# Kernel optimization log

Measured on AMD Instinct MI355X. Metric: run time of the kernel, lower is better.

Reference implementation:

```python
import jax, jax.numpy as jnp
import numpy as np

NUM_LAYERS = 5  # shared parameters across layers


def _crelu(z):
    # complex ReLU: ReLU applied independently to real and imag parts
    return jnp.maximum(z.real, 0.0) + 1j * jnp.maximum(z.imag, 0.0)


def _layer(Habs2, diagH, noise, maxpow, v, ar, dl, rc):
    # ---- u step ----
    # cov: [B,K,1] = |H|^2 @ |v|^2 (sum over last dim keepdim is identity for width-1) + noise
    cov = jnp.sum(Habs2 @ (jnp.abs(v) ** 2), axis=-1, keepdims=True) + noise[..., None]
    u = diagH[..., None] * v / cov  # [B,K,1] complex
    # ---- w step ---- (w_poly=None branch)
    err = 1.0 - jnp.conj(u) * diagH[..., None] * v
    w = 1.0 / err  # [B,K,1] complex
    # ---- v step ----
    v_tilde = jnp.conj(diagH)[..., None] * u * w  # [B,K,1]
    ul = (jnp.abs(u) ** 2) * jnp.abs(w)  # real [B,K,1]
    ul = jnp.sum(jnp.abs(jnp.swapaxes(Habs2, -2, -1) @ ul), axis=-1, keepdims=True)
    mu = jnp.maximum(jnp.abs(v_tilde) / jnp.sqrt(maxpow)[..., None] - ul, 0.0)
    ula = (ul + mu).astype(v_tilde.dtype)
    # ar + diagload branches: [B,K,1,1] @ [1,C] -> [B,K,1,C]
    vt = (v_tilde / ula)[..., None] @ ar + v_tilde[..., None] @ dl
    # nonlin + recombination: [B,K,1,C] @ [C,1] -> [B,K,1,1]
    vt = _crelu(vt) @ rc
    v_new = vt[..., 0]  # [B,K,1]
    # power correction
    cur = jnp.maximum(maxpow[..., None], jnp.abs(v_new) ** 2)
    corr = jnp.minimum(jnp.sqrt(maxpow[..., None] / cur), 1.0)
    return v_new * corr, u, w


def setup_inputs() -> dict:
    key = jax.random.key(0)
    ks = jax.random.split(key, 12)
    B, K, C = 64, 512, 4
    s = 1.0 / np.sqrt(C + 1)
    inp = {
        "h_re": jax.random.normal(ks[0], (B, K, K), jnp.float32),
        "h_im": jax.random.normal(ks[1], (B, K, K), jnp.float32),
        "user_noise_pow": jax.random.uniform(ks[2], (B, K), jnp.float32, 0.1, 1.0),
        "bss_maxpow": jnp.ones((B, K), jnp.float32),
        "v_in_re": jax.random.normal(ks[3], (B, K, 1), jnp.float32) * 0.5,
        "v_in_im": jax.random.normal(ks[4], (B, K, 1), jnp.float32) * 0.5,
        "ar_re": jax.random.normal(ks[5], (1, C), jnp.float32) * s,
        "ar_im": jax.random.normal(ks[6], (1, C), jnp.float32) * s,
        "dl_re": jax.random.normal(ks[7], (1, C), jnp.float32) * s,
        "dl_im": jax.random.normal(ks[8], (1, C), jnp.float32) * s,
        "rc_re": jax.random.normal(ks[9], (C, 1), jnp.float32) * s,
        "rc_im": jax.random.normal(ks[10], (C, 1), jnp.float32) * s,
    }
    return inp


def reference(h_re, h_im, user_noise_pow, bss_maxpow, v_in_re, v_in_im,
              ar_re, ar_im, dl_re, dl_im, rc_re, rc_im):
    H = (h_re + 1j * h_im).astype(jnp.complex64)
    Habs2 = h_re * h_re + h_im * h_im  # |H|^2, real [B,K,K]
    diagH = jnp.diagonal(H, axis1=-2, axis2=-1)  # [B,K]
    v = (v_in_re + 1j * v_in_im).astype(jnp.complex64)
    ar = (ar_re + 1j * ar_im).astype(jnp.complex64)
    dl = (dl_re + 1j * dl_im).astype(jnp.complex64)
    rc = (rc_re + 1j * rc_im).astype(jnp.complex64)
    vs = []
    for _ in range(NUM_LAYERS):
        v, u, w = _layer(Habs2, diagH, user_noise_pow, bss_maxpow, v, ar, dl, rc)
        vs.append(v)
    vstack = jnp.stack(vs, 0)  # [L,B,K,1] complex
    # return real/imag stacked so the output is a real tensor: [L,B,K,1,2]
    return jnp.stack([vstack.real, vstack.imag], axis=-1)
```

## Files before the change

### kernel.cpp

```cpp
#include <hip/hip_runtime.h>

#define B    64
#define K    512
#define C    4
#define NL   5
#define BK   (B*K)
#define ROWS 128
#define NT   1024
#define GRID (B*4)

typedef _Float16 half_t;
typedef _Float16 half8 __attribute__((ext_vector_type(8)));

#define PART_OFF   0
#define VST_OFF    (36*K*4)
#define XSQ_OFF    (VST_OFF + K*8)
#define MPL_OFF    (XSQ_OFF + K*4)
#define NZ_OFF     (MPL_OFF + K*4)
#define DAB_OFF    (NZ_OFF + ROWS*4)
#define SMEM_BYTES (DAB_OFF + ROWS*4)

__device__ __forceinline__ float ld_l3(const float* p) {
    return __uint_as_float(__hip_atomic_load((const unsigned*)p,
        __ATOMIC_RELAXED, __HIP_MEMORY_SCOPE_AGENT));
}
__device__ __forceinline__ void st_l3(float* p, float v) {
    __hip_atomic_store((unsigned*)p, __float_as_uint(v),
        __ATOMIC_RELAXED, __HIP_MEMORY_SCOPE_AGENT);
}
__device__ __forceinline__ void st_l3_2(float2* p, float2 v) {
    unsigned long long u = ((unsigned long long)__float_as_uint(v.y) << 32)
                         | (unsigned long long)__float_as_uint(v.x);
    __hip_atomic_store((unsigned long long*)p, u,
        __ATOMIC_RELAXED, __HIP_MEMORY_SCOPE_AGENT);
}
__device__ __forceinline__ float2 ld_l3_2(const float2* p) {
    unsigned long long u = __hip_atomic_load((const unsigned long long*)p,
        __ATOMIC_RELAXED, __HIP_MEMORY_SCOPE_AGENT);
    return make_float2(__uint_as_float((unsigned)(u & 0xffffffffu)),
                       __uint_as_float((unsigned)(u >> 32)));
}

template <int CTRL, int ROWMASK>
__device__ __forceinline__ float dppadd(float x) {
    int t = __builtin_amdgcn_update_dpp(0, __float_as_int(x), CTRL, ROWMASK,
                                        0xf, true);
    return x + __int_as_float(t);
}
__device__ __forceinline__ float wsum(float x) {
    x = dppadd<0x111, 0xf>(x);
    x = dppadd<0x112, 0xf>(x);
    x = dppadd<0x114, 0xf>(x);
    x = dppadd<0x118, 0xf>(x);
    x = dppadd<0x142, 0xa>(x);
    x = dppadd<0x143, 0xc>(x);
    return __int_as_float(__builtin_amdgcn_readlane(__float_as_int(x), 63));
}

__global__ __launch_bounds__(NT, 4) void k_all(
    const float* __restrict__ hre,  const float* __restrict__ him,
    const float* __restrict__ noise,const float* __restrict__ mp,
    const float* __restrict__ vre,  const float* __restrict__ vim,
    const float* __restrict__ ar_re,const float* __restrict__ ar_im,
    const float* __restrict__ dl_re,const float* __restrict__ dl_im,
    const float* __restrict__ rc_re,const float* __restrict__ rc_im,
    float2* __restrict__ vtilde,
    float*  __restrict__ ulpart,
    unsigned* __restrict__ bar,
    float* __restrict__ out)
{
    extern __shared__ char smem[];
    float*  part = (float*) (smem + PART_OFF);
    float2* vst  = (float2*)(smem + VST_OFF);
    float*  xsq  = (float*) (smem + XSQ_OFF);
    float*  mpl  = (float*) (smem + MPL_OFF);
    float*  nz   = (float*) (smem + NZ_OFF);
    float*  dab  = (float*) (smem + DAB_OFF);

    const int tid  = threadIdx.x;
    const int lane = tid & 63;
    const int w    = tid >> 6;
    const int b    = blockIdx.x & 63;
    const int q    = blockIdx.x >> 6;
    const int j0   = q * ROWS;
    unsigned* qb   = bar + ((unsigned)b << 5);

    if (tid < K) {
        float a = vre[b * K + tid], c2 = vim[b * K + tid];
        vst[tid] = make_float2(a, c2);
        xsq[tid] = a * a + c2 * c2;
        mpl[tid] = mp[b * K + tid];
    } else if (tid < K + ROWS) {
        nz[tid - K] = noise[b * K + j0 + (tid - K)];
    }
    __syncthreads();

    float xq[8];
#pragma unroll
    for (int t = 0; t < 8; ++t) xq[t] = xsq[t * 64 + lane];

    half8 h[8];
    float rs0[8];
    {
        const size_t gb = ((size_t)b * K + j0) * K;
        float ra[2][8], ia[2][8];
#pragma unroll
        for (int t = 0; t < 8; ++t) {
            ra[0][t] = __builtin_nontemporal_load(hre + gb + (size_t)w * K + t * 64 + lane);
            ia[0][t] = __builtin_nontemporal_load(him + gb + (size_t)w * K + t * 64 + lane);
        }
#pragma unroll
        for (int i = 0; i < 8; ++i) {
            const int cur = i & 1, nxt = cur ^ 1;
            if (i < 7) {
                const size_t rb = gb + (size_t)(16 * (i + 1) + w) * K;
#pragma unroll
                for (int t = 0; t < 8; ++t) {
                    ra[nxt][t] = __builtin_nontemporal_load(hre + rb + t * 64 + lane);
                    ia[nxt][t] = __builtin_nontemporal_load(him + rb + t * 64 + lane);
                }
            }
            float s[8], acc = 0.f;
            half8 hh;
#pragma unroll
            for (int t = 0; t < 8; ++t) {
                s[t]  = ra[cur][t] * ra[cur][t] + ia[cur][t] * ia[cur][t];
                hh[t] = (_Float16)s[t];
                acc  += s[t] * xq[t];
            }
            h[i] = hh;
            const int row = 16 * i + w;
            const int j   = j0 + row;
            if (lane == (j & 63)) dab[row] = s[j >> 6];
            rs0[i] = wsum(acc);
        }
    }

    for (int l = 0; l < NL; ++l) {
        const int buf = l & 1;
        float scov[8];
        if (l == 0) {
#pragma unroll
            for (int r = 0; r < 8; ++r) scov[r] = rs0[r];
        } else {
#pragma unroll
            for (int t = 0; t < 8; ++t) xq[t] = xsq[t * 64 + lane];
#pragma unroll
            for (int r = 0; r < 8; ++r) {
                float acc = 0.f;
#pragma unroll
                for (int t = 0; t < 8; ++t) acc += (float)h[r][t] * xq[t];
                scov[r] = wsum(acc);
            }
        }
        float ulv_own = 0.f;
        if (lane < 8) {
            float s = scov[0];
#pragma unroll
            for (int r = 1; r < 8; ++r) s = (lane == r) ? scov[r] : s;
            const int row = 16 * lane + w;
            const int j   = j0 + row;
            const int bj  = b * K + j;
            const float cov = s + nz[row];
            const float d2  = dab[row];
            const float A   = d2 * xsq[j];
            const float ww  = cov / (cov - A);
            const float sc  = d2 * ww / cov;
            const float2 vv = vst[j];
            st_l3_2(&vtilde[buf * BK + bj], make_float2(sc * vv.x, sc * vv.y));
            ulv_own = A * ww / (cov * cov);
        }
        float ulv[8];
#pragma unroll
        for (int r = 0; r < 8; ++r)
            ulv[r] = __int_as_float(
                __builtin_amdgcn_readlane(__float_as_int(ulv_own), r));

#pragma unroll
        for (int t = 0; t < 8; ++t) {
            float a = 0.f;
#pragma unroll
            for (int r = 0; r < 8; ++r) a += (float)h[r][t] * ulv[r];
            part[w * K + t * 64 + lane] = a;
        }
        __syncthreads();

        float s2 = 0.f;
        if (tid < K) {
#pragma unroll
            for (int ws2 = 0; ws2 < 16; ++ws2) s2 += part[ws2 * K + tid];
            st_l3(&ulpart[(size_t)buf * (B*4*K) + ((size_t)(b*4 + q)) * K + tid],
                  s2);
        }
        __syncthreads();
        if (tid == 0)
            __hip_atomic_fetch_add(qb, 1u, __ATOMIC_RELAXED,
                                   __HIP_MEMORY_SCOPE_AGENT);
        if (lane == 0) {
            const unsigned target = 4u * (unsigned)(l + 1);
            while (__hip_atomic_load(qb, __ATOMIC_RELAXED,
                                     __HIP_MEMORY_SCOPE_AGENT) < target)
                __builtin_amdgcn_s_sleep(2);
        }
        asm volatile("" ::: "memory");

        if (tid < K) {
            const int k  = tid;
            const int bk = b * K + k;
            const float* up = ulpart + (size_t)buf * (B*4*K) + (size_t)(b*4) * K;
            const float2 vt = ld_l3_2(&vtilde[buf * BK + bk]);
            float ul = s2;
#pragma unroll
            for (int qq = 0; qq < 4; ++qq)
                if (qq != q) ul += ld_l3(up + qq * K + k);
            const float p   = mpl[k];
            const float avt = sqrtf(vt.x*vt.x + vt.y*vt.y);
            const float mu  = fmaxf(avt / sqrtf(p) - ul, 0.f);
            const float inv = 1.f / (ul + mu);
            float ax = 0.f, ay = 0.f;
#pragma unroll
            for (int c = 0; c < C; ++c) {
                const float gre = ar_re[c] * inv + dl_re[c];
                const float gim = ar_im[c] * inv + dl_im[c];
                float zre = vt.x * gre - vt.y * gim;
                float zim = vt.x * gim + vt.y * gre;
                zre = fmaxf(zre, 0.f);
                zim = fmaxf(zim, 0.f);
                ax += zre * rc_re[c] - zim * rc_im[c];
                ay += zre * rc_im[c] + zim * rc_re[c];
            }
            const float n2   = ax*ax + ay*ay;
            const float cur  = fmaxf(p, n2);
            const float corr = fminf(sqrtf(p / cur), 1.f);
            ax *= corr; ay *= corr;
            if ((k >> 7) == q)
                ((float2*)out)[(size_t)l * BK + bk] = make_float2(ax, ay);
            vst[k] = make_float2(ax, ay);
            xsq[k] = ax * ax + ay * ay;
        }
        __syncthreads();
    }
}

extern "C" void kernel_launch(void* const* d_in, const int* in_sizes, int n_in,
                              void* d_out, int out_size, void* d_ws, size_t ws_size,
                              hipStream_t stream) {
    const float* hre   = (const float*)d_in[0];
    const float* him   = (const float*)d_in[1];
    const float* noise = (const float*)d_in[2];
    const float* mp    = (const float*)d_in[3];
    const float* vre   = (const float*)d_in[4];
    const float* vim   = (const float*)d_in[5];
    const float* ar_re = (const float*)d_in[6];
    const float* ar_im = (const float*)d_in[7];
    const float* dl_re = (const float*)d_in[8];
    const float* dl_im = (const float*)d_in[9];
    const float* rc_re = (const float*)d_in[10];
    const float* rc_im = (const float*)d_in[11];
    float* out = (float*)d_out;

    char*     ws     = (char*)d_ws;
    float2*   vtilde = (float2*)ws;
    float*    ulpart = (float*)(ws + 2*(size_t)BK*8);
    unsigned* bar    = (unsigned*)(ws + 2*(size_t)BK*8 + 2*(size_t)B*4*K*4);

    static bool attr_done = false;
    if (!attr_done) {
        (void)hipFuncSetAttribute((const void*)k_all,
                                  hipFuncAttributeMaxDynamicSharedMemorySize,
                                  SMEM_BYTES);
        attr_done = true;
    }

    (void)hipMemsetAsync(bar, 0, B * 32 * sizeof(unsigned), stream);

    hipLaunchKernelGGL(k_all, dim3(GRID), dim3(NT), SMEM_BYTES, stream,
                       hre, him, noise, mp, vre, vim,
                       ar_re, ar_im, dl_re, dl_im, rc_re, rc_im,
                       vtilde, ulpart, bar, out);
}
```

Measured before the change: 189.6 us.

## Split each batch across eight 512-thread blocks instead of four 1024-thread blocks

Work is repartitioned so each block handles 64 rows of H with 512 threads, and the grid doubles to 512 blocks. The per-batch barrier now waits for 8 arrivals, and the ul partial reduction sums 8 partial vectors. Shared memory is padded with a 36 KB dummy region, apparently to limit how many blocks share a CU. The goal is to spread the one-time load of H over more CUs for more memory parallelism. The cost is more inter-block partial traffic and a wider barrier.

```diff
diff --git a/kernel.cpp b/kernel.cpp
--- a/kernel.cpp
+++ b/kernel.cpp
@@ -5,20 +5,21 @@
 #define C    4
 #define NL   5
 #define BK   (B*K)
-#define ROWS 128
-#define NT   1024
-#define GRID (B*4)
+#define ROWS 64
+#define NT   512
+#define GRID (B*8)
 
 typedef _Float16 half_t;
 typedef _Float16 half8 __attribute__((ext_vector_type(8)));
 
 #define PART_OFF   0
-#define VST_OFF    (36*K*4)
+#define VST_OFF    (8*K*4)
 #define XSQ_OFF    (VST_OFF + K*8)
 #define MPL_OFF    (XSQ_OFF + K*4)
 #define NZ_OFF     (MPL_OFF + K*4)
 #define DAB_OFF    (NZ_OFF + ROWS*4)
-#define SMEM_BYTES (DAB_OFF + ROWS*4)
+#define PAD_OFF    (DAB_OFF + ROWS*4)
+#define SMEM_BYTES (PAD_OFF + 36864)
 
 __device__ __forceinline__ float ld_l3(const float* p) {
     return __uint_as_float(__hip_atomic_load((const unsigned*)p,
@@ -80,18 +81,17 @@
     const int tid  = threadIdx.x;
     const int lane = tid & 63;
     const int w    = tid >> 6;
-    const int b    = blockIdx.x & 63;
-    const int q    = blockIdx.x >> 6;
-    const int j0   = q * ROWS;
-    unsigned* qb   = bar + ((unsigned)b << 5);
-
-    if (tid < K) {
-        float a = vre[b * K + tid], c2 = vim[b * K + tid];
+    const int bt   = blockIdx.x >> 3;
+    const int oct  = blockIdx.x & 7;
+    const int j0   = oct * ROWS;
+    unsigned* qb   = bar + ((unsigned)bt << 5);
+
+    {
+        float a = vre[bt * K + tid], c2 = vim[bt * K + tid];
         vst[tid] = make_float2(a, c2);
         xsq[tid] = a * a + c2 * c2;
-        mpl[tid] = mp[b * K + tid];
-    } else if (tid < K + ROWS) {
-        nz[tid - K] = noise[b * K + j0 + (tid - K)];
+        mpl[tid] = mp[bt * K + tid];
+        if (tid < ROWS) nz[tid] = noise[bt * K + j0 + tid];
     }
     __syncthreads();
 
@@ -102,7 +102,7 @@
     half8 h[8];
     float rs0[8];
     {
-        const size_t gb = ((size_t)b * K + j0) * K;
+        const size_t gb = ((size_t)bt * K + j0) * K;
         float ra[2][8], ia[2][8];
 #pragma unroll
         for (int t = 0; t < 8; ++t) {
@@ -113,7 +113,7 @@
         for (int i = 0; i < 8; ++i) {
             const int cur = i & 1, nxt = cur ^ 1;
             if (i < 7) {
-                const size_t rb = gb + (size_t)(16 * (i + 1) + w) * K;
+                const size_t rb = gb + (size_t)(8 * (i + 1) + w) * K;
 #pragma unroll
                 for (int t = 0; t < 8; ++t) {
                     ra[nxt][t] = __builtin_nontemporal_load(hre + rb + t * 64 + lane);
@@ -129,7 +129,7 @@
                 acc  += s[t] * xq[t];
             }
             h[i] = hh;
-            const int row = 16 * i + w;
+            const int row = 8 * i + w;
             const int j   = j0 + row;
             if (lane == (j & 63)) dab[row] = s[j >> 6];
             rs0[i] = wsum(acc);
@@ -158,9 +158,9 @@
             float s = scov[0];
 #pragma unroll
             for (int r = 1; r < 8; ++r) s = (lane == r) ? scov[r] : s;
-            const int row = 16 * lane + w;
+            const int row = 8 * lane + w;
             const int j   = j0 + row;
-            const int bj  = b * K + j;
+            const int bj  = bt * K + j;
             const float cov = s + nz[row];
             const float d2  = dab[row];
             const float A   = d2 * xsq[j];
@@ -186,33 +186,31 @@
         __syncthreads();
 
         float s2 = 0.f;
-        if (tid < K) {
-#pragma unroll
-            for (int ws2 = 0; ws2 < 16; ++ws2) s2 += part[ws2 * K + tid];
-            st_l3(&ulpart[(size_t)buf * (B*4*K) + ((size_t)(b*4 + q)) * K + tid],
-                  s2);
-        }
+#pragma unroll
+        for (int ws2 = 0; ws2 < 8; ++ws2) s2 += part[ws2 * K + tid];
+        st_l3(&ulpart[(size_t)buf * (B*8*K) + ((size_t)(bt*8 + oct)) * K + tid],
+              s2);
         __syncthreads();
         if (tid == 0)
             __hip_atomic_fetch_add(qb, 1u, __ATOMIC_RELAXED,
                                    __HIP_MEMORY_SCOPE_AGENT);
         if (lane == 0) {
-            const unsigned target = 4u * (unsigned)(l + 1);
+            const unsigned target = 8u * (unsigned)(l + 1);
             while (__hip_atomic_load(qb, __ATOMIC_RELAXED,
                                      __HIP_MEMORY_SCOPE_AGENT) < target)
                 __builtin_amdgcn_s_sleep(2);
         }
         asm volatile("" ::: "memory");
 
-        if (tid < K) {
+        {
             const int k  = tid;
-            const int bk = b * K + k;
-            const float* up = ulpart + (size_t)buf * (B*4*K) + (size_t)(b*4) * K;
+            const int bk = bt * K + k;
+            const float* up = ulpart + (size_t)buf * (B*8*K) + (size_t)(bt*8) * K;
             const float2 vt = ld_l3_2(&vtilde[buf * BK + bk]);
             float ul = s2;
 #pragma unroll
-            for (int qq = 0; qq < 4; ++qq)
-                if (qq != q) ul += ld_l3(up + qq * K + k);
+            for (int oo = 0; oo < 8; ++oo)
+                if (oo != oct) ul += ld_l3(up + oo * K + k);
             const float p   = mpl[k];
             const float avt = sqrtf(vt.x*vt.x + vt.y*vt.y);
             const float mu  = fmaxf(avt / sqrtf(p) - ul, 0.f);
@@ -233,7 +231,7 @@
             const float cur  = fmaxf(p, n2);
             const float corr = fminf(sqrtf(p / cur), 1.f);
             ax *= corr; ay *= corr;
-            if ((k >> 7) == q)
+            if ((k >> 6) == oct)
                 ((float2*)out)[(size_t)l * BK + bk] = make_float2(ax, ay);
             vst[k] = make_float2(ax, ay);
             xsq[k] = ax * ax + ay * ay;
@@ -262,7 +260,7 @@
     char*     ws     = (char*)d_ws;
     float2*   vtilde = (float2*)ws;
     float*    ulpart = (float*)(ws + 2*(size_t)BK*8);
-    unsigned* bar    = (unsigned*)(ws + 2*(size_t)BK*8 + 2*(size_t)B*4*K*4);
+    unsigned* bar    = (unsigned*)(ws + 2*(size_t)BK*8 + 2*(size_t)B*8*K*4);
 
     static bool attr_done = false;
     if (!attr_done) {
```

Result: slower. 196.2 us (+3.5%).

## Replace per-batch counter barrier with tagged per-element flag exchange of partial sums

Applied to the files above, without the earlier changes.

Drops the atomic counter barrier and its extra __syncthreads between blocks of the same batch. Each partial-sum element is now written as a (value, layer-tag) 64-bit pair, and consumers spin on the tag of the individual elements they need. The intent is to remove barrier latency and the serialised counter round-trips, at the cost of a larger memset of the exchange buffer and per-thread polling. Loads of H also switch from nontemporal to normal loads.

```diff
diff --git a/kernel.cpp b/kernel.cpp
--- a/kernel.cpp
+++ b/kernel.cpp
@@ -24,10 +24,6 @@
     return __uint_as_float(__hip_atomic_load((const unsigned*)p,
         __ATOMIC_RELAXED, __HIP_MEMORY_SCOPE_AGENT));
 }
-__device__ __forceinline__ void st_l3(float* p, float v) {
-    __hip_atomic_store((unsigned*)p, __float_as_uint(v),
-        __ATOMIC_RELAXED, __HIP_MEMORY_SCOPE_AGENT);
-}
 __device__ __forceinline__ void st_l3_2(float2* p, float2 v) {
     unsigned long long u = ((unsigned long long)__float_as_uint(v.y) << 32)
                          | (unsigned long long)__float_as_uint(v.x);
@@ -65,8 +61,7 @@
     const float* __restrict__ dl_re,const float* __restrict__ dl_im,
     const float* __restrict__ rc_re,const float* __restrict__ rc_im,
     float2* __restrict__ vtilde,
-    float*  __restrict__ ulpart,
-    unsigned* __restrict__ bar,
+    float2* __restrict__ ulpart,
     float* __restrict__ out)
 {
     extern __shared__ char smem[];
@@ -83,7 +78,6 @@
     const int b    = blockIdx.x & 63;
     const int q    = blockIdx.x >> 6;
     const int j0   = q * ROWS;
-    unsigned* qb   = bar + ((unsigned)b << 5);
 
     if (tid < K) {
         float a = vre[b * K + tid], c2 = vim[b * K + tid];
@@ -106,8 +100,8 @@
         float ra[2][8], ia[2][8];
 #pragma unroll
         for (int t = 0; t < 8; ++t) {
-            ra[0][t] = __builtin_nontemporal_load(hre + gb + (size_t)w * K + t * 64 + lane);
-            ia[0][t] = __builtin_nontemporal_load(him + gb + (size_t)w * K + t * 64 + lane);
+            ra[0][t] = hre[gb + (size_t)w * K + t * 64 + lane];
+            ia[0][t] = him[gb + (size_t)w * K + t * 64 + lane];
         }
 #pragma unroll
         for (int i = 0; i < 8; ++i) {
@@ -116,8 +110,8 @@
                 const size_t rb = gb + (size_t)(16 * (i + 1) + w) * K;
 #pragma unroll
                 for (int t = 0; t < 8; ++t) {
-                    ra[nxt][t] = __builtin_nontemporal_load(hre + rb + t * 64 + lane);
-                    ia[nxt][t] = __builtin_nontemporal_load(him + rb + t * 64 + lane);
+                    ra[nxt][t] = hre[rb + t * 64 + lane];
+                    ia[nxt][t] = him[rb + t * 64 + lane];
                 }
             }
             float s[8], acc = 0.f;
@@ -138,6 +132,7 @@
 
     for (int l = 0; l < NL; ++l) {
         const int buf = l & 1;
+        const unsigned tag = (unsigned)(l + 1);
         float scov[8];
         if (l == 0) {
 #pragma unroll
@@ -189,30 +184,33 @@
         if (tid < K) {
 #pragma unroll
             for (int ws2 = 0; ws2 < 16; ++ws2) s2 += part[ws2 * K + tid];
-            st_l3(&ulpart[(size_t)buf * (B*4*K) + ((size_t)(b*4 + q)) * K + tid],
-                  s2);
-        }
-        __syncthreads();
-        if (tid == 0)
-            __hip_atomic_fetch_add(qb, 1u, __ATOMIC_RELAXED,
-                                   __HIP_MEMORY_SCOPE_AGENT);
-        if (lane == 0) {
-            const unsigned target = 4u * (unsigned)(l + 1);
-            while (__hip_atomic_load(qb, __ATOMIC_RELAXED,
-                                     __HIP_MEMORY_SCOPE_AGENT) < target)
-                __builtin_amdgcn_s_sleep(2);
+            st_l3_2(&ulpart[(size_t)buf * (B*4*K) + ((size_t)(b*4 + q)) * K + tid],
+                    make_float2(s2, __uint_as_float(tag)));
         }
         asm volatile("" ::: "memory");
 
         if (tid < K) {
             const int k  = tid;
             const int bk = b * K + k;
-            const float* up = ulpart + (size_t)buf * (B*4*K) + (size_t)(b*4) * K;
+            const float2* up = ulpart + (size_t)buf * (B*4*K) + (size_t)(b*4) * K;
+            const int q1 = (q + 1) & 3, q2 = (q + 2) & 3, q3 = (q + 3) & 3;
+            float2 va = ld_l3_2(up + q1 * K + k);
+            float2 vb = ld_l3_2(up + q2 * K + k);
+            float2 vc = ld_l3_2(up + q3 * K + k);
+            while (__float_as_uint(va.y) != tag) {
+                __builtin_amdgcn_s_sleep(1);
+                va = ld_l3_2(up + q1 * K + k);
+            }
+            while (__float_as_uint(vb.y) != tag) {
+                __builtin_amdgcn_s_sleep(1);
+                vb = ld_l3_2(up + q2 * K + k);
+            }
+            while (__float_as_uint(vc.y) != tag) {
+                __builtin_amdgcn_s_sleep(1);
+                vc = ld_l3_2(up + q3 * K + k);
+            }
+            float ul = s2 + va.x + vb.x + vc.x;
             const float2 vt = ld_l3_2(&vtilde[buf * BK + bk]);
-            float ul = s2;
-#pragma unroll
-            for (int qq = 0; qq < 4; ++qq)
-                if (qq != q) ul += ld_l3(up + qq * K + k);
             const float p   = mpl[k];
             const float avt = sqrtf(vt.x*vt.x + vt.y*vt.y);
             const float mu  = fmaxf(avt / sqrtf(p) - ul, 0.f);
@@ -259,10 +257,9 @@
     const float* rc_im = (const float*)d_in[11];
     float* out = (float*)d_out;
 
-    char*     ws     = (char*)d_ws;
-    float2*   vtilde = (float2*)ws;
-    float*    ulpart = (float*)(ws + 2*(size_t)BK*8);
-    unsigned* bar    = (unsigned*)(ws + 2*(size_t)BK*8 + 2*(size_t)B*4*K*4);
+    char*   ws     = (char*)d_ws;
+    float2* vtilde = (float2*)ws;
+    float2* ulpart = (float2*)(ws + 2*(size_t)BK*8);
 
     static bool attr_done = false;
     if (!attr_done) {
@@ -272,10 +269,10 @@
         attr_done = true;
     }
 
-    (void)hipMemsetAsync(bar, 0, B * 32 * sizeof(unsigned), stream);
+    (void)hipMemsetAsync(ulpart, 0, 2*(size_t)(B*4)*K*sizeof(float2), stream);
 
     hipLaunchKernelGGL(k_all, dim3(GRID), dim3(NT), SMEM_BYTES, stream,
                        hre, him, noise, mp, vre, vim,
                        ar_re, ar_im, dl_re, dl_im, rc_re, rc_im,
-                       vtilde, ulpart, bar, out);
-}
+                       vtilde, ulpart, out);
+}
```

Result: no change. 193.2 us (+1.9%).
